# Optimization experiments

Hardware: AMD Instinct MI355X
Metric: run time of the kernel (lower is better)

Reference implementation:

```python
import jax, jax.numpy as jnp
import numpy as np

EMBED_DIM = 1024
NUM_HEADS = 16
HEAD_DIM = EMBED_DIM // NUM_HEADS


def setup_inputs() -> dict:
    key = jax.random.key(0)
    k1, k2, k3 = jax.random.split(key, 3)
    B, S = 4, 2048
    scale = 1.0 / np.sqrt(EMBED_DIM)
    x = jax.random.normal(k1, (B, S, EMBED_DIM), dtype=jnp.float32)
    w_qkv = jax.random.normal(k2, (EMBED_DIM, 3 * EMBED_DIM), dtype=jnp.float32) * scale
    b_qkv = jnp.zeros((3 * EMBED_DIM,), dtype=jnp.float32)
    w_proj = jax.random.normal(k3, (EMBED_DIM, EMBED_DIM), dtype=jnp.float32) * scale
    b_proj = jnp.zeros((EMBED_DIM,), dtype=jnp.float32)
    return {"x": x, "w_qkv": w_qkv, "b_qkv": b_qkv, "w_proj": w_proj, "b_proj": b_proj}


def reference(x, w_qkv, b_qkv, w_proj, b_proj):
    # x: [B, S, E]. Dropout is identity in eval mode.
    B, S, E = x.shape
    qkv = x @ w_qkv + b_qkv                                  # [B, S, 3E]
    qkv = qkv.reshape(B, S, 3, NUM_HEADS, HEAD_DIM)
    qkv = jnp.transpose(qkv, (2, 0, 3, 1, 4))                # [3, B, H, S, Dh]
    q, k, v = qkv[0], qkv[1], qkv[2]
    scores = jnp.einsum("bhsd,bhtd->bhst", q, k) / np.sqrt(HEAD_DIM)
    probs = jax.nn.softmax(scores, axis=-1)                  # [B, H, S, S]
    out = jnp.einsum("bhst,bhtd->bhsd", probs, v)            # [B, H, S, Dh]
    out = jnp.transpose(out, (0, 2, 1, 3)).reshape(B, S, E)
    return out @ w_proj + b_proj
```

## Files before the change

kernel.cpp:

```cpp
#include <hip/hip_runtime.h>

typedef unsigned short u16;
typedef __bf16 bf16x8_v __attribute__((ext_vector_type(8)));
typedef unsigned short u16x8 __attribute__((ext_vector_type(8)));
typedef unsigned short u16x4 __attribute__((ext_vector_type(4)));
typedef unsigned short u16x2 __attribute__((ext_vector_type(2)));
typedef float f32x4 __attribute__((ext_vector_type(4)));

typedef const __attribute__((address_space(1))) void* gas_ptr;
typedef __attribute__((address_space(3))) void* las_ptr;

static __device__ __forceinline__ u16 f2bf(float f) {
  unsigned int u = __builtin_bit_cast(unsigned int, f);
  u = (u + 0x7fffu + ((u >> 16) & 1u)) >> 16;
  return (u16)u;
}

static __device__ __forceinline__ f32x4 mfma16(u16x8 a, u16x8 b, f32x4 c) {
  return __builtin_amdgcn_mfma_f32_16x16x32_bf16(
      __builtin_bit_cast(bf16x8_v, a), __builtin_bit_cast(bf16x8_v, b), c, 0, 0, 0);
}

static __device__ __forceinline__ void gload_lds16(const u16* g, u16* lds) {
  __builtin_amdgcn_global_load_lds((gas_ptr)g, (las_ptr)lds, 16, 0, 0);
}

__global__ __launch_bounds__(256) void cvt_bf16(const float* __restrict__ in,
                                                u16* __restrict__ out, int n4) {
  int i = blockIdx.x * 256 + threadIdx.x;
  if (i >= n4) return;
  float4 v = ((const float4*)in)[i];
  ushort4 o;
  o.x = f2bf(v.x); o.y = f2bf(v.y); o.z = f2bf(v.z); o.w = f2bf(v.w);
  ((ushort4*)out)[i] = o;
}

__global__ __launch_bounds__(256) void transpose_cvt(const float* __restrict__ w,
                                                     u16* __restrict__ wt, int K, int N) {
  __shared__ float t[32][33];
  const int n0 = blockIdx.x * 32, k0 = blockIdx.y * 32;
  const int tx = threadIdx.x & 31, ty = threadIdx.x >> 5;
#pragma unroll
  for (int i = 0; i < 4; ++i) {
    int k = ty + i * 8;
    t[k][tx] = w[(size_t)(k0 + k) * N + n0 + tx];
  }
  __syncthreads();
#pragma unroll
  for (int i = 0; i < 4; ++i) {
    int n = ty + i * 8;
    wt[(size_t)(n0 + n) * K + k0 + tx] = f2bf(t[tx][n]);
  }
}

template <bool BF16_OUT>
__global__ __launch_bounds__(256)
void gemm_bt(const u16* __restrict__ A, const u16* __restrict__ Bt,
             const float* __restrict__ bias, void* __restrict__ Cv,
             int M, int N, int K) {
  __shared__ u16 As[128 * 32];
  __shared__ u16 Bs[128 * 32];
  const int tid = threadIdx.x;
  const int l = tid & 63, w = tid >> 6;
  const int lr = l & 15, lg = l >> 4;
  const int wr = w >> 1, wc = w & 1;
  const int m0 = blockIdx.y * 128, n0 = blockIdx.x * 128;

  f32x4 acc[4][4];
#pragma unroll
  for (int i = 0; i < 4; ++i)
#pragma unroll
    for (int j = 0; j < 4; ++j) acc[i][j] = f32x4{0.f, 0.f, 0.f, 0.f};

  for (int ks = 0; ks < K; ks += 32) {
#pragma unroll
    for (int i = 0; i < 2; ++i) {
      const int c = i * 256 + w * 64 + l;
      const int row = c >> 2, kc = (c & 3) << 3;
      gload_lds16(A + (size_t)(m0 + row) * K + ks + kc, &As[(i * 256 + w * 64) * 8]);
      gload_lds16(Bt + (size_t)(n0 + row) * K + ks + kc, &Bs[(i * 256 + w * 64) * 8]);
    }
    __syncthreads();
    u16x8 af[4], bfr[4];
#pragma unroll
    for (int m = 0; m < 4; ++m)
      af[m] = *(const u16x8*)&As[(wr * 64 + m * 16 + lr) * 32 + lg * 8];
#pragma unroll
    for (int n = 0; n < 4; ++n)
      bfr[n] = *(const u16x8*)&Bs[(wc * 64 + n * 16 + lr) * 32 + lg * 8];
#pragma unroll
    for (int m = 0; m < 4; ++m)
#pragma unroll
      for (int n = 0; n < 4; ++n)
        acc[m][n] = mfma16(af[m], bfr[n], acc[m][n]);
    __syncthreads();
  }

#pragma unroll
  for (int m = 0; m < 4; ++m) {
    const int grow = m0 + wr * 64 + m * 16 + lg * 4;
#pragma unroll
    for (int n = 0; n < 4; ++n) {
      const int gcol = n0 + wc * 64 + n * 16 + lr;
      const float bv = bias[gcol];
#pragma unroll
      for (int r = 0; r < 4; ++r) {
        const float v = acc[m][n][r] + bv;
        if (BF16_OUT)
          ((u16*)Cv)[(size_t)(grow + r) * N + gcol] = f2bf(v);
        else
          ((float*)Cv)[(size_t)(grow + r) * N + gcol] = v;
      }
    }
  }
}

__global__ __launch_bounds__(256)
void attn64(const u16* __restrict__ qkv, u16* __restrict__ ctx) {
  constexpr int S = 2048, E3 = 3072, E = 1024;
  __shared__ u16 Ks[64 * 64];
  __shared__ u16 Vt[64 * 64];
  char* KsB = (char*)Ks;
  char* VtB = (char*)Vt;
  const int tid = threadIdx.x, l = tid & 63, w = tid >> 6;
  const int lr = l & 15, lg = l >> 4;
  const int qt = blockIdx.x, bh = blockIdx.y;
  const int b = bh >> 4, h = bh & 15;
  const u16* base = qkv + (size_t)b * S * E3;
  const int qcol = h * 64, kcol = E + h * 64, vcol = 2 * E + h * 64;
  const int s0 = qt * 64;
  const float C2 = 0.1803368801f;

  u16x8 qf[2];
  {
    const u16* qp = base + (size_t)(s0 + w * 16 + lr) * E3 + qcol + lg * 8;
    qf[0] = *(const u16x8*)qp;
    qf[1] = *(const u16x8*)(qp + 32);
  }

  f32x4 o[4];
#pragma unroll
  for (int d = 0; d < 4; ++d) o[d] = f32x4{0.f, 0.f, 0.f, 0.f};
  float M2 = -1e30f;
  float lsum = 0.f;

  for (int kt = 0; kt < S; kt += 64) {
    __syncthreads();
#pragma unroll
    for (int i = 0; i < 2; ++i) {
      const int c = i * 256 + tid;
      const int t = c >> 3, dby = (c & 7) << 4;
      u16x8 kv = *(const u16x8*)&base[(size_t)(kt + t) * E3 + kcol + ((c & 7) << 3)];
      *(u16x8*)&KsB[t * 128 + (dby ^ ((t & 7) << 4))] = kv;
    }
    {
      const int tp = tid >> 3, d0 = (tid & 7) << 3;
      const int t0 = tp * 2;
      const u16* vp = base + (size_t)(kt + t0) * E3 + vcol + d0;
      u16x8 v0 = *(const u16x8*)vp;
      u16x8 v1 = *(const u16x8*)(vp + E3);
#pragma unroll
      for (int e = 0; e < 8; ++e) {
        const int row = d0 + e;
        u16x2 pr;
        pr[0] = v0[e];
        pr[1] = v1[e];
        *(u16x2*)&VtB[row * 128 + ((tp * 4) ^ ((row & 15) << 3))] = pr;
      }
    }
    __syncthreads();

    f32x4 sacc[4];
#pragma unroll
    for (int tf = 0; tf < 4; ++tf) sacc[tf] = f32x4{0.f, 0.f, 0.f, 0.f};
#pragma unroll
    for (int kk = 0; kk < 2; ++kk)
#pragma unroll
      for (int tf = 0; tf < 4; ++tf) {
        const int row = tf * 16 + lr;
        u16x8 kf = *(const u16x8*)&KsB[row * 128 + ((kk * 64 + lg * 16) ^ ((row & 7) << 4))];
        sacc[tf] = mfma16(kf, qf[kk], sacc[tf]);
      }

    float mx = fmaxf(
        fmaxf(fmaxf(fmaxf(sacc[0][0], sacc[0][1]), fmaxf(sacc[0][2], sacc[0][3])),
              fmaxf(fmaxf(sacc[1][0], sacc[1][1]), fmaxf(sacc[1][2], sacc[1][3]))),
        fmaxf(fmaxf(fmaxf(sacc[2][0], sacc[2][1]), fmaxf(sacc[2][2], sacc[2][3])),
              fmaxf(fmaxf(sacc[3][0], sacc[3][1]), fmaxf(sacc[3][2], sacc[3][3]))));
    mx = fmaxf(mx, __shfl_xor(mx, 16, 64));
    mx = fmaxf(mx, __shfl_xor(mx, 32, 64));
    const float M2new = fmaxf(M2, mx * C2);
    const float alpha = exp2f(M2 - M2new);
#pragma unroll
    for (int tf = 0; tf < 4; ++tf)
#pragma unroll
      for (int r = 0; r < 4; ++r)
        sacc[tf][r] = exp2f(fmaf(sacc[tf][r], C2, -M2new));
    float ps = ((sacc[0][0] + sacc[0][1]) + (sacc[0][2] + sacc[0][3])) +
               ((sacc[1][0] + sacc[1][1]) + (sacc[1][2] + sacc[1][3])) +
               ((sacc[2][0] + sacc[2][1]) + (sacc[2][2] + sacc[2][3])) +
               ((sacc[3][0] + sacc[3][1]) + (sacc[3][2] + sacc[3][3]));
    ps += __shfl_xor(ps, 16, 64);
    ps += __shfl_xor(ps, 32, 64);
    lsum = lsum * alpha + ps;
    M2 = M2new;
    if (__any(alpha != 1.0f)) {
      float ar[4];
#pragma unroll
      for (int r = 0; r < 4; ++r) ar[r] = __shfl(alpha, 4 * lg + r, 64);
#pragma unroll
      for (int dt = 0; dt < 4; ++dt)
#pragma unroll
        for (int r = 0; r < 4; ++r) o[dt][r] *= ar[r];
    }

#pragma unroll
    for (int kk = 0; kk < 2; ++kk) {
      u16x8 pa;
#pragma unroll
      for (int e = 0; e < 8; ++e) pa[e] = f2bf(sacc[2 * kk + (e >> 2)][e & 3]);
#pragma unroll
      for (int dt = 0; dt < 4; ++dt) {
        const int row = dt * 16 + lr;
        const int cb = kk * 64 + lg * 8;
        const int sw = (row & 15) << 3;
        u16x4 vlo = *(const u16x4*)&VtB[row * 128 + (cb ^ sw)];
        u16x4 vhi = *(const u16x4*)&VtB[row * 128 + ((cb + 32) ^ sw)];
        u16x8 vf = __builtin_shufflevector(vlo, vhi, 0, 1, 2, 3, 4, 5, 6, 7);
        o[dt] = mfma16(pa, vf, o[dt]);
      }
    }
  }

  const float linv = 1.0f / lsum;
#pragma unroll
  for (int r = 0; r < 4; ++r) {
    const float ir = __shfl(linv, 4 * lg + r, 64);
    const int row = s0 + w * 16 + 4 * lg + r;
    const size_t rb = ((size_t)b * S + row) * E + h * 64;
#pragma unroll
    for (int dt = 0; dt < 4; ++dt) ctx[rb + dt * 16 + lr] = f2bf(o[dt][r] * ir);
  }
}

extern "C" void kernel_launch(void* const* d_in, const int* in_sizes, int n_in,
                              void* d_out, int out_size, void* d_ws, size_t ws_size,
                              hipStream_t stream) {
  const float* x = (const float*)d_in[0];
  const float* w_qkv = (const float*)d_in[1];
  const float* b_qkv = (const float*)d_in[2];
  const float* w_proj = (const float*)d_in[3];
  const float* b_proj = (const float*)d_in[4];
  float* out = (float*)d_out;

  const int B = 4, S = 2048, E = 1024;

  const size_t E2 = (size_t)E * E, SE = (size_t)S * E;
  int NB = 1;
  if (ws_size >= 2 * (4 * E2 + 16 * SE)) NB = 4;
  else if (ws_size >= 2 * (4 * E2 + 8 * SE)) NB = 2;

  u16* ws = (u16*)d_ws;
  u16* wqkvt = ws;
  u16* wprojt = wqkvt + 3 * E2;
  u16* xbf   = wprojt + E2;
  u16* qkvb  = xbf + (size_t)NB * SE;
  u16* ctx   = xbf;

  transpose_cvt<<<dim3(3 * E / 32, E / 32), 256, 0, stream>>>(w_qkv, wqkvt, E, 3 * E);
  transpose_cvt<<<dim3(E / 32, E / 32), 256, 0, stream>>>(w_proj, wprojt, E, E);

  for (int g = 0; g < B; g += NB) {
    const int Mg = NB * S;
    const float* xg = x + (size_t)g * SE;
    float* outg = out + (size_t)g * SE;
    cvt_bf16<<<(Mg * E / 4 + 255) / 256, 256, 0, stream>>>(xg, xbf, Mg * E / 4);
    gemm_bt<true><<<dim3(3 * E / 128, Mg / 128), 256, 0, stream>>>(xbf, wqkvt, b_qkv, qkvb, Mg, 3 * E, E);
    attn64<<<dim3(S / 64, NB * 16), 256, 0, stream>>>(qkvb, ctx);
    gemm_bt<false><<<dim3(E / 128, Mg / 128), 256, 0, stream>>>(ctx, wprojt, b_proj, outg, Mg, E, E);
  }
}
```

Baseline: 372.7 us.

## Compute softmax row sums via MFMA with ones vector and async K loads

The attention kernel now accumulates the softmax denominator with an extra MFMA against a ones column instead of a shuffle-based sum reduction. It also loads K tiles straight into LDS with global_load_lds, swizzling the source address rather than the destination. P and output conversion now use a native bf16 cast instead of manual rounding. The aim is to cut VALU, shuffle and register-staging work in the inner loop. The cost is one extra MFMA per half-tile, and the row sums now come from bf16-rounded probabilities, which changes numerics slightly.

```diff
diff --git a/kernel.cpp b/kernel.cpp
--- a/kernel.cpp
+++ b/kernel.cpp
@@ -19,6 +19,10 @@
 static __device__ __forceinline__ f32x4 mfma16(u16x8 a, u16x8 b, f32x4 c) {
   return __builtin_amdgcn_mfma_f32_16x16x32_bf16(
       __builtin_bit_cast(bf16x8_v, a), __builtin_bit_cast(bf16x8_v, b), c, 0, 0, 0);
+}
+
+static __device__ __forceinline__ f32x4 mfma16v(bf16x8_v a, bf16x8_v b, f32x4 c) {
+  return __builtin_amdgcn_mfma_f32_16x16x32_bf16(a, b, c, 0, 0, 0);
 }
 
 static __device__ __forceinline__ void gload_lds16(const u16* g, u16* lds) {
@@ -131,6 +135,14 @@
   const int s0 = qt * 64;
   const float C2 = 0.1803368801f;
 
+  bf16x8_v onesv;
+  {
+    u16x8 ou;
+#pragma unroll
+    for (int e = 0; e < 8; ++e) ou[e] = (lr == 0) ? (u16)0x3F80 : (u16)0;
+    onesv = __builtin_bit_cast(bf16x8_v, ou);
+  }
+
   u16x8 qf[2];
   {
     const u16* qp = base + (size_t)(s0 + w * 16 + lr) * E3 + qcol + lg * 8;
@@ -141,17 +153,18 @@
   f32x4 o[4];
 #pragma unroll
   for (int d = 0; d < 4; ++d) o[d] = f32x4{0.f, 0.f, 0.f, 0.f};
+  f32x4 ls = f32x4{0.f, 0.f, 0.f, 0.f};
   float M2 = -1e30f;
-  float lsum = 0.f;
 
   for (int kt = 0; kt < S; kt += 64) {
     __syncthreads();
 #pragma unroll
     for (int i = 0; i < 2; ++i) {
       const int c = i * 256 + tid;
-      const int t = c >> 3, dby = (c & 7) << 4;
-      u16x8 kv = *(const u16x8*)&base[(size_t)(kt + t) * E3 + kcol + ((c & 7) << 3)];
-      *(u16x8*)&KsB[t * 128 + (dby ^ ((t & 7) << 4))] = kv;
+      const int t = c >> 3;
+      const int sc = ((c & 7) ^ (t & 7)) << 3;
+      gload_lds16(base + (size_t)(kt + t) * E3 + kcol + sc,
+                  &Ks[(i * 256 + w * 64) * 8]);
     }
     {
       const int tp = tid >> 3, d0 = (tid & 7) << 3;
@@ -182,11 +195,12 @@
         sacc[tf] = mfma16(kf, qf[kk], sacc[tf]);
       }
 
-    float mx = fmaxf(
-        fmaxf(fmaxf(fmaxf(sacc[0][0], sacc[0][1]), fmaxf(sacc[0][2], sacc[0][3])),
-              fmaxf(fmaxf(sacc[1][0], sacc[1][1]), fmaxf(sacc[1][2], sacc[1][3]))),
-        fmaxf(fmaxf(fmaxf(sacc[2][0], sacc[2][1]), fmaxf(sacc[2][2], sacc[2][3])),
-              fmaxf(fmaxf(sacc[3][0], sacc[3][1]), fmaxf(sacc[3][2], sacc[3][3]))));
+    float m0 = fmaxf(fmaxf(sacc[0][0], sacc[0][1]), sacc[0][2]);
+    float m1 = fmaxf(fmaxf(sacc[0][3], sacc[1][0]), sacc[1][1]);
+    float m2 = fmaxf(fmaxf(sacc[1][2], sacc[1][3]), sacc[2][0]);
+    float m3 = fmaxf(fmaxf(sacc[2][1], sacc[2][2]), sacc[2][3]);
+    float m4 = fmaxf(fmaxf(sacc[3][0], sacc[3][1]), sacc[3][2]);
+    float mx = fmaxf(fmaxf(fmaxf(m0, m1), m2), fmaxf(fmaxf(m3, m4), sacc[3][3]));
     mx = fmaxf(mx, __shfl_xor(mx, 16, 64));
     mx = fmaxf(mx, __shfl_xor(mx, 32, 64));
     const float M2new = fmaxf(M2, mx * C2);
@@ -196,13 +210,6 @@
 #pragma unroll
       for (int r = 0; r < 4; ++r)
         sacc[tf][r] = exp2f(fmaf(sacc[tf][r], C2, -M2new));
-    float ps = ((sacc[0][0] + sacc[0][1]) + (sacc[0][2] + sacc[0][3])) +
-               ((sacc[1][0] + sacc[1][1]) + (sacc[1][2] + sacc[1][3])) +
-               ((sacc[2][0] + sacc[2][1]) + (sacc[2][2] + sacc[2][3])) +
-               ((sacc[3][0] + sacc[3][1]) + (sacc[3][2] + sacc[3][3]));
-    ps += __shfl_xor(ps, 16, 64);
-    ps += __shfl_xor(ps, 32, 64);
-    lsum = lsum * alpha + ps;
     M2 = M2new;
     if (__any(alpha != 1.0f)) {
       float ar[4];
@@ -212,13 +219,15 @@
       for (int dt = 0; dt < 4; ++dt)
 #pragma unroll
         for (int r = 0; r < 4; ++r) o[dt][r] *= ar[r];
+#pragma unroll
+      for (int r = 0; r < 4; ++r) ls[r] *= ar[r];
     }
 
 #pragma unroll
     for (int kk = 0; kk < 2; ++kk) {
-      u16x8 pa;
-#pragma unroll
-      for (int e = 0; e < 8; ++e) pa[e] = f2bf(sacc[2 * kk + (e >> 2)][e & 3]);
+      bf16x8_v pav;
+#pragma unroll
+      for (int e = 0; e < 8; ++e) pav[e] = (__bf16)sacc[2 * kk + (e >> 2)][e & 3];
 #pragma unroll
       for (int dt = 0; dt < 4; ++dt) {
         const int row = dt * 16 + lr;
@@ -226,20 +235,23 @@
         const int sw = (row & 15) << 3;
         u16x4 vlo = *(const u16x4*)&VtB[row * 128 + (cb ^ sw)];
         u16x4 vhi = *(const u16x4*)&VtB[row * 128 + ((cb + 32) ^ sw)];
-        u16x8 vf = __builtin_shufflevector(vlo, vhi, 0, 1, 2, 3, 4, 5, 6, 7);
-        o[dt] = mfma16(pa, vf, o[dt]);
-      }
-    }
-  }
-
-  const float linv = 1.0f / lsum;
+        bf16x8_v vf = __builtin_bit_cast(bf16x8_v,
+            __builtin_shufflevector(vlo, vhi, 0, 1, 2, 3, 4, 5, 6, 7));
+        o[dt] = mfma16v(pav, vf, o[dt]);
+      }
+      ls = mfma16v(pav, onesv, ls);
+    }
+  }
+
 #pragma unroll
   for (int r = 0; r < 4; ++r) {
-    const float ir = __shfl(linv, 4 * lg + r, 64);
+    const float den = __shfl(ls[r], l & 48, 64);
+    const float ir = 1.0f / den;
     const int row = s0 + w * 16 + 4 * lg + r;
     const size_t rb = ((size_t)b * S + row) * E + h * 64;
 #pragma unroll
-    for (int dt = 0; dt < 4; ++dt) ctx[rb + dt * 16 + lr] = f2bf(o[dt][r] * ir);
+    for (int dt = 0; dt < 4; ++dt)
+      ctx[rb + dt * 16 + lr] = __builtin_bit_cast(u16, (__bf16)(o[dt][r] * ir));
   }
 }
 
```

After: 363.4 us. -2.5%, faster.
